# Performance work log

Hardware: AMD Instinct MI355X
Metric: run time of the kernel (lower is better)

The kernel has to match this reference:

```python
import jax, jax.numpy as jnp
import numpy as np

COMMITMENT_COST = 0.25
NUM_EMBEDDINGS = 8192
EMBEDDING_DIM = 64


def setup_inputs() -> dict:
    key = jax.random.key(0)
    k1, k2 = jax.random.split(key)
    z_e = jax.random.normal(k1, (32, 1024, EMBEDDING_DIM), dtype=jnp.float32)
    # nn.Embedding init: uniform(-1/num_embeddings, 1/num_embeddings)
    lim = 1.0 / NUM_EMBEDDINGS
    weight = jax.random.uniform(k2, (NUM_EMBEDDINGS, EMBEDDING_DIM), dtype=jnp.float32,
                                minval=-lim, maxval=lim)
    return {"z_e": z_e, "weight": weight}


def reference(z_e, weight):
    B = z_e.shape[0]
    D = weight.shape[1]
    z_flat = z_e.reshape(-1, D)  # [T, D], T = B*N
    # squared euclidean distances: ||z||^2 + ||e||^2 - 2 z e^T  -> [T, K]
    distances = (jnp.sum(z_flat ** 2, axis=1, keepdims=True)
                 + jnp.sum(weight ** 2, axis=1)
                 - 2.0 * jnp.matmul(z_flat, weight.T))
    encoding_indices = jnp.argmin(distances, axis=1)  # [T]
    # direct gather == one-hot @ weight (same math, no dense one-hot)
    z_q = weight[encoding_indices].reshape(z_e.shape)
    loss_1 = jnp.mean((jax.lax.stop_gradient(z_e) - z_q) ** 2)
    loss_2 = jnp.mean((z_e - jax.lax.stop_gradient(z_q)) ** 2)
    vq_loss = loss_1 + COMMITMENT_COST * loss_2
    # straight-through estimator
    z_q_st = z_e + jax.lax.stop_gradient(z_q - z_e)
    return (z_q_st, vq_loss)
```

## Files before the change

### kernel.cpp

```cpp
#include <hip/hip_runtime.h>

typedef float f32x16 __attribute__((ext_vector_type(16)));

#define NUM_EMB 8192
#define DIM 64
#define NTOK 32768
#define TOKS_PER_BLOCK 64
#define TOK_BLOCKS 512
#define ESPLIT 4
#define CHUNKS_PER_WAVE 16

#define B_SCALE (-8192.0f)
#define SCORE_BIAS 128.0f

#define WSB_OFF  0
#define WSA_OFF  (512 * 1024)
#define GKEY_OFF (WSA_OFF + 2 * 1024 * 1024)
#define CNT_OFF  (GKEY_OFF + 128 * 1024)
#define CNT2_OFF (CNT_OFF + 2048)
#define LOSSW_OFF (CNT2_OFF + 4)

__device__ __forceinline__ unsigned umin2(unsigned a, unsigned b) { return a < b ? a : b; }

__global__ __launch_bounds__(256) void vq_prep(const float* __restrict__ z_e,
                                               const float* __restrict__ weight,
                                               uint4* __restrict__ wsB,
                                               uint2* __restrict__ wsA,
                                               unsigned* __restrict__ gkeys,
                                               unsigned* __restrict__ cnt,
                                               unsigned* __restrict__ cnt2,
                                               float* __restrict__ lossw) {
  int m = blockIdx.x * 256 + threadIdx.x;
  if (m < TOK_BLOCKS)
    __hip_atomic_store(&cnt[m], 0u, __ATOMIC_RELAXED, __HIP_MEMORY_SCOPE_AGENT);
  if (m == TOK_BLOCKS) {
    __hip_atomic_store(cnt2, 0u, __ATOMIC_RELAXED, __HIP_MEMORY_SCOPE_AGENT);
    __hip_atomic_store(lossw, 0.0f, __ATOMIC_RELAXED, __HIP_MEMORY_SCOPE_AGENT);
  }
  if (m < NUM_EMB * 4) {
    __hip_atomic_store(&gkeys[m], 0xFFFFFFFFu, __ATOMIC_RELAXED, __HIP_MEMORY_SCOPE_AGENT);
    int lane = m & 63, h = (m >> 6) & 1, c = m >> 7;
    int n = c * 32 + (lane & 31);
    int kb = (lane >> 5) * 8;
    const float* p = weight + n * DIM;
    unsigned r[4];
#pragma unroll
    for (int q = 0; q < 2; ++q) {
      const float* pk = p + (2 * h + q) * 16 + kb;
      int lo = __builtin_amdgcn_cvt_pk_fp8_f32(B_SCALE * pk[0], B_SCALE * pk[1], 0, false);
      lo     = __builtin_amdgcn_cvt_pk_fp8_f32(B_SCALE * pk[2], B_SCALE * pk[3], lo, true);
      int hi = __builtin_amdgcn_cvt_pk_fp8_f32(B_SCALE * pk[4], B_SCALE * pk[5], 0, false);
      hi     = __builtin_amdgcn_cvt_pk_fp8_f32(B_SCALE * pk[6], B_SCALE * pk[7], hi, true);
      r[q * 2] = (unsigned)lo; r[q * 2 + 1] = (unsigned)hi;
    }
    wsB[m] = make_uint4(r[0], r[1], r[2], r[3]);
  } else {
    int s = m - NUM_EMB * 4;
    int lane = s & 63, f = (s >> 6) & 3, tr = (s >> 8) & 1, tile = s >> 9;
    int token = tile * 64 + tr * 32 + (lane & 31);
    const float* p = z_e + (size_t)token * DIM + f * 16 + (lane >> 5) * 8;
    int lo = __builtin_amdgcn_cvt_pk_fp8_f32(p[0], p[1], 0, false);
    lo     = __builtin_amdgcn_cvt_pk_fp8_f32(p[2], p[3], lo, true);
    int hi = __builtin_amdgcn_cvt_pk_fp8_f32(p[4], p[5], 0, false);
    hi     = __builtin_amdgcn_cvt_pk_fp8_f32(p[6], p[7], hi, true);
    wsA[s] = make_uint2((unsigned)lo, (unsigned)hi);
  }
}

__global__ __launch_bounds__(256, 4) void vq_main(const float* __restrict__ z_e,
                                                  const float* __restrict__ weight,
                                                  const uint2* __restrict__ wsA,
                                                  const uint4* __restrict__ wsB,
                                                  unsigned* __restrict__ gkeys,
                                                  unsigned* __restrict__ cnt,
                                                  unsigned* __restrict__ cnt2,
                                                  float* __restrict__ lossw,
                                                  float* __restrict__ out,
                                                  float* __restrict__ loss_out) {
  __shared__ unsigned lds_part[4][64];
  __shared__ unsigned lds_tok[64];
  __shared__ float wsum[4];
  __shared__ int winner;
  __shared__ int final_blk;

  const int tid  = threadIdx.x;
  const int lane = tid & 63;
  const int wave = tid >> 6;
  const int half = lane >> 5;
  const int ln31 = lane & 31;
  const int tblk = blockIdx.x & (TOK_BLOCKS - 1);
  const int eblk = blockIdx.x >> 9;
  const int tbase = tblk * TOKS_PER_BLOCK;

  long long afrag[2][4];
#pragma unroll
  for (int tr = 0; tr < 2; ++tr)
#pragma unroll
    for (int f = 0; f < 4; ++f) {
      uint2 u = wsA[(size_t)(((tblk * 2 + tr) * 4 + f) * 64 + lane)];
      __builtin_memcpy(&afrag[tr][f], &u, 8);
    }

  f32x16 bias;
#pragma unroll
  for (int i = 0; i < 16; ++i) bias[i] = SCORE_BIAS;

  unsigned run0[16], run1[16];
#pragma unroll
  for (int i = 0; i < 16; ++i) { run0[i] = 0xFFFFFFFFu; run1[i] = 0xFFFFFFFFu; }

  const int c0 = eblk * (CHUNKS_PER_WAVE * 4) + wave * CHUNKS_PER_WAVE;
  unsigned idx = (unsigned)(c0 * 32 + ln31);

  uint4 bA = wsB[(c0 * 2 + 0) * 64 + lane];
  uint4 bB = wsB[(c0 * 2 + 1) * 64 + lane];

  for (int c = 0; c < CHUNKS_PER_WAVE; ++c) {
    int cn = (c == CHUNKS_PER_WAVE - 1) ? c0 : (c0 + c + 1);
    uint4 nA = wsB[(cn * 2 + 0) * 64 + lane];
    uint4 nB = wsB[(cn * 2 + 1) * 64 + lane];

    long long b0, b1, b2, b3;
    __builtin_memcpy(&b0, &bA.x, 8);
    __builtin_memcpy(&b1, &bA.z, 8);
    __builtin_memcpy(&b2, &bB.x, 8);
    __builtin_memcpy(&b3, &bB.z, 8);

    f32x16 acc0 = __builtin_amdgcn_mfma_f32_32x32x16_fp8_fp8(afrag[0][0], b0, bias, 0, 0, 0);
    f32x16 acc1 = __builtin_amdgcn_mfma_f32_32x32x16_fp8_fp8(afrag[1][0], b0, bias, 0, 0, 0);
    acc0 = __builtin_amdgcn_mfma_f32_32x32x16_fp8_fp8(afrag[0][1], b1, acc0, 0, 0, 0);
    acc1 = __builtin_amdgcn_mfma_f32_32x32x16_fp8_fp8(afrag[1][1], b1, acc1, 0, 0, 0);
    acc0 = __builtin_amdgcn_mfma_f32_32x32x16_fp8_fp8(afrag[0][2], b2, acc0, 0, 0, 0);
    acc1 = __builtin_amdgcn_mfma_f32_32x32x16_fp8_fp8(afrag[1][2], b2, acc1, 0, 0, 0);
    acc0 = __builtin_amdgcn_mfma_f32_32x32x16_fp8_fp8(afrag[0][3], b3, acc0, 0, 0, 0);
    acc1 = __builtin_amdgcn_mfma_f32_32x32x16_fp8_fp8(afrag[1][3], b3, acc1, 0, 0, 0);

#pragma unroll
    for (int i = 0; i < 16; ++i) {
      run0[i] = umin2(run0[i], (__float_as_uint(acc0[i]) & 0xFFFFE000u) | idx);
      run1[i] = umin2(run1[i], (__float_as_uint(acc1[i]) & 0xFFFFE000u) | idx);
    }
    idx += 32;
    bA = nA; bB = nB;
  }

#pragma unroll
  for (int i = 0; i < 16; ++i) {
    unsigned v = run0[i];
    v = umin2(v, (unsigned)__builtin_amdgcn_ds_swizzle((int)v, 0x041F));
    v = umin2(v, (unsigned)__builtin_amdgcn_ds_swizzle((int)v, 0x081F));
    v = umin2(v, (unsigned)__builtin_amdgcn_ds_swizzle((int)v, 0x101F));
    v = umin2(v, (unsigned)__builtin_amdgcn_ds_swizzle((int)v, 0x201F));
    v = umin2(v, (unsigned)__builtin_amdgcn_ds_swizzle((int)v, 0x401F));
    run0[i] = v;
    unsigned w = run1[i];
    w = umin2(w, (unsigned)__builtin_amdgcn_ds_swizzle((int)w, 0x041F));
    w = umin2(w, (unsigned)__builtin_amdgcn_ds_swizzle((int)w, 0x081F));
    w = umin2(w, (unsigned)__builtin_amdgcn_ds_swizzle((int)w, 0x101F));
    w = umin2(w, (unsigned)__builtin_amdgcn_ds_swizzle((int)w, 0x201F));
    w = umin2(w, (unsigned)__builtin_amdgcn_ds_swizzle((int)w, 0x401F));
    run1[i] = w;
  }

  if (ln31 == 0) {
#pragma unroll
    for (int reg = 0; reg < 16; ++reg) {
      int rowl = (reg & 3) + 8 * (reg >> 2) + 4 * half;
      lds_part[wave][rowl]      = run0[reg];
      lds_part[wave][32 + rowl] = run1[reg];
    }
  }
  __syncthreads();

  if (tid < 64) {
    unsigned k = umin2(umin2(lds_part[0][tid], lds_part[1][tid]),
                       umin2(lds_part[2][tid], lds_part[3][tid]));
    atomicMin(&gkeys[tbase + tid], k);
  }
  __syncthreads();

  if (tid == 0) {
    unsigned prev = __hip_atomic_fetch_add(&cnt[tblk], 1u, __ATOMIC_RELAXED,
                                           __HIP_MEMORY_SCOPE_AGENT);
    winner = (prev == ESPLIT - 1);
  }
  __syncthreads();

  if (winner) {
    if (tid < 64)
      lds_tok[tid] = __hip_atomic_load(&gkeys[tbase + tid], __ATOMIC_RELAXED,
                                       __HIP_MEMORY_SCOPE_AGENT) & 0x1FFFu;
    __syncthreads();
    const float4* z4 = reinterpret_cast<const float4*>(z_e);
    const float4* w4 = reinterpret_cast<const float4*>(weight);
    float4* o4 = reinterpret_cast<float4*>(out);
    float lsum = 0.0f;
#pragma unroll
    for (int r = 0; r < 4; ++r) {
      int g = r * 256 + tid;
      int t = g >> 4, q = g & 15;
      float4 z = z4[(size_t)tbase * 16 + g];
      float4 w = w4[(size_t)lds_tok[t] * 16 + q];
      float4 o;
      o.x = z.x + (w.x - z.x); o.y = z.y + (w.y - z.y);
      o.z = z.z + (w.z - z.z); o.w = z.w + (w.w - z.w);
      o4[(size_t)tbase * 16 + g] = o;
      float dx = z.x - w.x, dy = z.y - w.y, dz = z.z - w.z, dw = z.w - w.w;
      lsum += dx * dx + dy * dy + dz * dz + dw * dw;
    }
#pragma unroll
    for (int s = 32; s >= 1; s >>= 1) lsum += __shfl_xor(lsum, s, 64);
    if (lane == 0) wsum[wave] = lsum;
    __syncthreads();
    if (tid == 0)
      atomicAdd(lossw, (wsum[0] + wsum[1] + wsum[2] + wsum[3]) * (1.25f / 2097152.0f));
    __syncthreads();
    if (tid == 0) {
      unsigned p2 = __hip_atomic_fetch_add(cnt2, 1u, __ATOMIC_RELAXED,
                                           __HIP_MEMORY_SCOPE_AGENT);
      final_blk = (p2 == TOK_BLOCKS - 1);
    }
    __syncthreads();
    if (final_blk && tid == 0)
      *loss_out = __hip_atomic_load(lossw, __ATOMIC_RELAXED, __HIP_MEMORY_SCOPE_AGENT);
  }
}

extern "C" void kernel_launch(void* const* d_in, const int* in_sizes, int n_in,
                              void* d_out, int out_size, void* d_ws, size_t ws_size,
                              hipStream_t stream) {
  const float* z_e    = (const float*)d_in[0];
  const float* weight = (const float*)d_in[1];
  float* out  = (float*)d_out;
  float* loss = out + (out_size - 1);
  char* ws = (char*)d_ws;
  uint4* wsB = (uint4*)(ws + WSB_OFF);
  uint2* wsA = (uint2*)(ws + WSA_OFF);
  unsigned* gkeys = (unsigned*)(ws + GKEY_OFF);
  unsigned* cnt   = (unsigned*)(ws + CNT_OFF);
  unsigned* cnt2  = (unsigned*)(ws + CNT2_OFF);
  float* lossw    = (float*)(ws + LOSSW_OFF);

  vq_prep<<<1152, 256, 0, stream>>>(z_e, weight, wsB, wsA, gkeys, cnt, cnt2, lossw);
  vq_main<<<TOK_BLOCKS * ESPLIT, 256, 0, stream>>>(z_e, weight, wsA, wsB, gkeys, cnt,
                                                   cnt2, lossw, out, loss);
}
```

Measured before the change: 107.6 us.

## Drop codebook split; each block scans full codebook for 32 tokens

```diff
diff --git a/kernel.cpp b/kernel.cpp
--- a/kernel.cpp
+++ b/kernel.cpp
@@ -5,111 +5,84 @@
 #define NUM_EMB 8192
 #define DIM 64
 #define NTOK 32768
-#define TOKS_PER_BLOCK 64
-#define TOK_BLOCKS 512
-#define ESPLIT 4
-#define CHUNKS_PER_WAVE 16
+#define TOKS_PER_BLOCK 32
+#define TOK_BLOCKS 1024
+#define CHUNKS_PER_WAVE 64
 
 #define B_SCALE (-8192.0f)
 #define SCORE_BIAS 128.0f
 
-#define WSB_OFF  0
-#define WSA_OFF  (512 * 1024)
-#define GKEY_OFF (WSA_OFF + 2 * 1024 * 1024)
-#define CNT_OFF  (GKEY_OFF + 128 * 1024)
-#define CNT2_OFF (CNT_OFF + 2048)
-#define LOSSW_OFF (CNT2_OFF + 4)
-
 __device__ __forceinline__ unsigned umin2(unsigned a, unsigned b) { return a < b ? a : b; }
 
-__global__ __launch_bounds__(256) void vq_prep(const float* __restrict__ z_e,
-                                               const float* __restrict__ weight,
+__global__ __launch_bounds__(256) void vq_prep(const float* __restrict__ weight,
                                                uint4* __restrict__ wsB,
-                                               uint2* __restrict__ wsA,
-                                               unsigned* __restrict__ gkeys,
-                                               unsigned* __restrict__ cnt,
-                                               unsigned* __restrict__ cnt2,
-                                               float* __restrict__ lossw) {
+                                               float* __restrict__ loss_out) {
   int m = blockIdx.x * 256 + threadIdx.x;
-  if (m < TOK_BLOCKS)
-    __hip_atomic_store(&cnt[m], 0u, __ATOMIC_RELAXED, __HIP_MEMORY_SCOPE_AGENT);
-  if (m == TOK_BLOCKS) {
-    __hip_atomic_store(cnt2, 0u, __ATOMIC_RELAXED, __HIP_MEMORY_SCOPE_AGENT);
-    __hip_atomic_store(lossw, 0.0f, __ATOMIC_RELAXED, __HIP_MEMORY_SCOPE_AGENT);
+  if (m == 0)
+    __hip_atomic_store(loss_out, 0.0f, __ATOMIC_RELAXED, __HIP_MEMORY_SCOPE_AGENT);
+  int lane = m & 63, h = (m >> 6) & 1, c = m >> 7;
+  int n = c * 32 + (lane & 31);
+  int kb = (lane >> 5) * 8;
+  const float* p = weight + n * DIM;
+  unsigned r[4];
+#pragma unroll
+  for (int q = 0; q < 2; ++q) {
+    const float* pk = p + (2 * h + q) * 16 + kb;
+    int lo = __builtin_amdgcn_cvt_pk_fp8_f32(B_SCALE * pk[0], B_SCALE * pk[1], 0, false);
+    lo     = __builtin_amdgcn_cvt_pk_fp8_f32(B_SCALE * pk[2], B_SCALE * pk[3], lo, true);
+    int hi = __builtin_amdgcn_cvt_pk_fp8_f32(B_SCALE * pk[4], B_SCALE * pk[5], 0, false);
+    hi     = __builtin_amdgcn_cvt_pk_fp8_f32(B_SCALE * pk[6], B_SCALE * pk[7], hi, true);
+    r[q * 2] = (unsigned)lo; r[q * 2 + 1] = (unsigned)hi;
   }
-  if (m < NUM_EMB * 4) {
-    __hip_atomic_store(&gkeys[m], 0xFFFFFFFFu, __ATOMIC_RELAXED, __HIP_MEMORY_SCOPE_AGENT);
-    int lane = m & 63, h = (m >> 6) & 1, c = m >> 7;
-    int n = c * 32 + (lane & 31);
-    int kb = (lane >> 5) * 8;
-    const float* p = weight + n * DIM;
-    unsigned r[4];
-#pragma unroll
-    for (int q = 0; q < 2; ++q) {
-      const float* pk = p + (2 * h + q) * 16 + kb;
-      int lo = __builtin_amdgcn_cvt_pk_fp8_f32(B_SCALE * pk[0], B_SCALE * pk[1], 0, false);
-      lo     = __builtin_amdgcn_cvt_pk_fp8_f32(B_SCALE * pk[2], B_SCALE * pk[3], lo, true);
-      int hi = __builtin_amdgcn_cvt_pk_fp8_f32(B_SCALE * pk[4], B_SCALE * pk[5], 0, false);
-      hi     = __builtin_amdgcn_cvt_pk_fp8_f32(B_SCALE * pk[6], B_SCALE * pk[7], hi, true);
-      r[q * 2] = (unsigned)lo; r[q * 2 + 1] = (unsigned)hi;
-    }
-    wsB[m] = make_uint4(r[0], r[1], r[2], r[3]);
-  } else {
-    int s = m - NUM_EMB * 4;
-    int lane = s & 63, f = (s >> 6) & 3, tr = (s >> 8) & 1, tile = s >> 9;
-    int token = tile * 64 + tr * 32 + (lane & 31);
-    const float* p = z_e + (size_t)token * DIM + f * 16 + (lane >> 5) * 8;
-    int lo = __builtin_amdgcn_cvt_pk_fp8_f32(p[0], p[1], 0, false);
-    lo     = __builtin_amdgcn_cvt_pk_fp8_f32(p[2], p[3], lo, true);
-    int hi = __builtin_amdgcn_cvt_pk_fp8_f32(p[4], p[5], 0, false);
-    hi     = __builtin_amdgcn_cvt_pk_fp8_f32(p[6], p[7], hi, true);
-    wsA[s] = make_uint2((unsigned)lo, (unsigned)hi);
-  }
+  wsB[m] = make_uint4(r[0], r[1], r[2], r[3]);
 }
 
 __global__ __launch_bounds__(256, 4) void vq_main(const float* __restrict__ z_e,
                                                   const float* __restrict__ weight,
-                                                  const uint2* __restrict__ wsA,
                                                   const uint4* __restrict__ wsB,
-                                                  unsigned* __restrict__ gkeys,
-                                                  unsigned* __restrict__ cnt,
-                                                  unsigned* __restrict__ cnt2,
-                                                  float* __restrict__ lossw,
                                                   float* __restrict__ out,
                                                   float* __restrict__ loss_out) {
-  __shared__ unsigned lds_part[4][64];
-  __shared__ unsigned lds_tok[64];
+  __shared__ unsigned char lds_a[TOKS_PER_BLOCK * 72];
+  __shared__ unsigned lds_part[4][TOKS_PER_BLOCK];
+  __shared__ unsigned lds_tok[TOKS_PER_BLOCK];
   __shared__ float wsum[4];
-  __shared__ int winner;
-  __shared__ int final_blk;
 
   const int tid  = threadIdx.x;
   const int lane = tid & 63;
   const int wave = tid >> 6;
   const int half = lane >> 5;
   const int ln31 = lane & 31;
-  const int tblk = blockIdx.x & (TOK_BLOCKS - 1);
-  const int eblk = blockIdx.x >> 9;
-  const int tbase = tblk * TOKS_PER_BLOCK;
+  const int tbase = blockIdx.x * TOKS_PER_BLOCK;
 
-  long long afrag[2][4];
+  {
+    int token = tid >> 3, g = tid & 7;
+    const float* p = z_e + (size_t)(tbase + token) * DIM + g * 8;
+    float4 x0 = *reinterpret_cast<const float4*>(p);
+    float4 x1 = *reinterpret_cast<const float4*>(p + 4);
+    int lo = __builtin_amdgcn_cvt_pk_fp8_f32(x0.x, x0.y, 0, false);
+    lo     = __builtin_amdgcn_cvt_pk_fp8_f32(x0.z, x0.w, lo, true);
+    int hi = __builtin_amdgcn_cvt_pk_fp8_f32(x1.x, x1.y, 0, false);
+    hi     = __builtin_amdgcn_cvt_pk_fp8_f32(x1.z, x1.w, hi, true);
+    *reinterpret_cast<uint2*>(&lds_a[token * 72 + g * 8]) = make_uint2((unsigned)lo, (unsigned)hi);
+  }
+  __syncthreads();
+
+  long long afrag[4];
 #pragma unroll
-  for (int tr = 0; tr < 2; ++tr)
-#pragma unroll
-    for (int f = 0; f < 4; ++f) {
-      uint2 u = wsA[(size_t)(((tblk * 2 + tr) * 4 + f) * 64 + lane)];
-      __builtin_memcpy(&afrag[tr][f], &u, 8);
-    }
+  for (int f = 0; f < 4; ++f) {
+    uint2 u = *reinterpret_cast<const uint2*>(&lds_a[ln31 * 72 + f * 16 + half * 8]);
+    __builtin_memcpy(&afrag[f], &u, 8);
+  }
 
   f32x16 bias;
 #pragma unroll
   for (int i = 0; i < 16; ++i) bias[i] = SCORE_BIAS;
 
-  unsigned run0[16], run1[16];
+  unsigned run[16];
 #pragma unroll
-  for (int i = 0; i < 16; ++i) { run0[i] = 0xFFFFFFFFu; run1[i] = 0xFFFFFFFFu; }
+  for (int i = 0; i < 16; ++i) run[i] = 0xFFFFFFFFu;
 
-  const int c0 = eblk * (CHUNKS_PER_WAVE * 4) + wave * CHUNKS_PER_WAVE;
+  const int c0 = wave * CHUNKS_PER_WAVE;
   unsigned idx = (unsigned)(c0 * 32 + ln31);
 
   uint4 bA = wsB[(c0 * 2 + 0) * 64 + lane];
@@ -126,104 +99,68 @@
     __builtin_memcpy(&b2, &bB.x, 8);
     __builtin_memcpy(&b3, &bB.z, 8);
 
-    f32x16 acc0 = __builtin_amdgcn_mfma_f32_32x32x16_fp8_fp8(afrag[0][0], b0, bias, 0, 0, 0);
-    f32x16 acc1 = __builtin_amdgcn_mfma_f32_32x32x16_fp8_fp8(afrag[1][0], b0, bias, 0, 0, 0);
-    acc0 = __builtin_amdgcn_mfma_f32_32x32x16_fp8_fp8(afrag[0][1], b1, acc0, 0, 0, 0);
-    acc1 = __builtin_amdgcn_mfma_f32_32x32x16_fp8_fp8(afrag[1][1], b1, acc1, 0, 0, 0);
-    acc0 = __builtin_amdgcn_mfma_f32_32x32x16_fp8_fp8(afrag[0][2], b2, acc0, 0, 0, 0);
-    acc1 = __builtin_amdgcn_mfma_f32_32x32x16_fp8_fp8(afrag[1][2], b2, acc1, 0, 0, 0);
-    acc0 = __builtin_amdgcn_mfma_f32_32x32x16_fp8_fp8(afrag[0][3], b3, acc0, 0, 0, 0);
-    acc1 = __builtin_amdgcn_mfma_f32_32x32x16_fp8_fp8(afrag[1][3], b3, acc1, 0, 0, 0);
+    f32x16 acc = __builtin_amdgcn_mfma_f32_32x32x16_fp8_fp8(afrag[0], b0, bias, 0, 0, 0);
+    acc = __builtin_amdgcn_mfma_f32_32x32x16_fp8_fp8(afrag[1], b1, acc, 0, 0, 0);
+    acc = __builtin_amdgcn_mfma_f32_32x32x16_fp8_fp8(afrag[2], b2, acc, 0, 0, 0);
+    acc = __builtin_amdgcn_mfma_f32_32x32x16_fp8_fp8(afrag[3], b3, acc, 0, 0, 0);
 
 #pragma unroll
-    for (int i = 0; i < 16; ++i) {
-      run0[i] = umin2(run0[i], (__float_as_uint(acc0[i]) & 0xFFFFE000u) | idx);
-      run1[i] = umin2(run1[i], (__float_as_uint(acc1[i]) & 0xFFFFE000u) | idx);
-    }
+    for (int i = 0; i < 16; ++i)
+      run[i] = umin2(run[i], (__float_as_uint(acc[i]) & 0xFFFFE000u) | idx);
     idx += 32;
     bA = nA; bB = nB;
   }
 
 #pragma unroll
   for (int i = 0; i < 16; ++i) {
-    unsigned v = run0[i];
+    unsigned v = run[i];
     v = umin2(v, (unsigned)__builtin_amdgcn_ds_swizzle((int)v, 0x041F));
     v = umin2(v, (unsigned)__builtin_amdgcn_ds_swizzle((int)v, 0x081F));
     v = umin2(v, (unsigned)__builtin_amdgcn_ds_swizzle((int)v, 0x101F));
     v = umin2(v, (unsigned)__builtin_amdgcn_ds_swizzle((int)v, 0x201F));
     v = umin2(v, (unsigned)__builtin_amdgcn_ds_swizzle((int)v, 0x401F));
-    run0[i] = v;
-    unsigned w = run1[i];
-    w = umin2(w, (unsigned)__builtin_amdgcn_ds_swizzle((int)w, 0x041F));
-    w = umin2(w, (unsigned)__builtin_amdgcn_ds_swizzle((int)w, 0x081F));
-    w = umin2(w, (unsigned)__builtin_amdgcn_ds_swizzle((int)w, 0x101F));
-    w = umin2(w, (unsigned)__builtin_amdgcn_ds_swizzle((int)w, 0x201F));
-    w = umin2(w, (unsigned)__builtin_amdgcn_ds_swizzle((int)w, 0x401F));
-    run1[i] = w;
+    run[i] = v;
   }
 
   if (ln31 == 0) {
 #pragma unroll
     for (int reg = 0; reg < 16; ++reg) {
-      int rowl = (reg & 3) + 8 * (reg >> 2) + 4 * half;
-      lds_part[wave][rowl]      = run0[reg];
-      lds_part[wave][32 + rowl] = run1[reg];
+      int row = (reg & 3) + 8 * (reg >> 2) + 4 * half;
+      lds_part[wave][row] = run[reg];
     }
   }
   __syncthreads();
 
-  if (tid < 64) {
+  if (tid < TOKS_PER_BLOCK) {
     unsigned k = umin2(umin2(lds_part[0][tid], lds_part[1][tid]),
                        umin2(lds_part[2][tid], lds_part[3][tid]));
-    atomicMin(&gkeys[tbase + tid], k);
+    lds_tok[tid] = k & 0x1FFFu;
   }
   __syncthreads();
 
-  if (tid == 0) {
-    unsigned prev = __hip_atomic_fetch_add(&cnt[tblk], 1u, __ATOMIC_RELAXED,
-                                           __HIP_MEMORY_SCOPE_AGENT);
-    winner = (prev == ESPLIT - 1);
+  const float4* z4 = reinterpret_cast<const float4*>(z_e);
+  const float4* w4 = reinterpret_cast<const float4*>(weight);
+  float4* o4 = reinterpret_cast<float4*>(out);
+  float lsum = 0.0f;
+#pragma unroll
+  for (int r = 0; r < 2; ++r) {
+    int g = r * 256 + tid;
+    int t = g >> 4, q = g & 15;
+    float4 z = z4[(size_t)tbase * 16 + g];
+    float4 w = w4[(size_t)lds_tok[t] * 16 + q];
+    float4 o;
+    o.x = z.x + (w.x - z.x); o.y = z.y + (w.y - z.y);
+    o.z = z.z + (w.z - z.z); o.w = z.w + (w.w - z.w);
+    o4[(size_t)tbase * 16 + g] = o;
+    float dx = z.x - w.x, dy = z.y - w.y, dz = z.z - w.z, dw = z.w - w.w;
+    lsum += dx * dx + dy * dy + dz * dz + dw * dw;
   }
+#pragma unroll
+  for (int s = 32; s >= 1; s >>= 1) lsum += __shfl_xor(lsum, s, 64);
+  if (lane == 0) wsum[wave] = lsum;
   __syncthreads();
-
-  if (winner) {
-    if (tid < 64)
-      lds_tok[tid] = __hip_atomic_load(&gkeys[tbase + tid], __ATOMIC_RELAXED,
-                                       __HIP_MEMORY_SCOPE_AGENT) & 0x1FFFu;
-    __syncthreads();
-    const float4* z4 = reinterpret_cast<const float4*>(z_e);
-    const float4* w4 = reinterpret_cast<const float4*>(weight);
-    float4* o4 = reinterpret_cast<float4*>(out);
-    float lsum = 0.0f;
-#pragma unroll
-    for (int r = 0; r < 4; ++r) {
-      int g = r * 256 + tid;
-      int t = g >> 4, q = g & 15;
-      float4 z = z4[(size_t)tbase * 16 + g];
-      float4 w = w4[(size_t)lds_tok[t] * 16 + q];
-      float4 o;
-      o.x = z.x + (w.x - z.x); o.y = z.y + (w.y - z.y);
-      o.z = z.z + (w.z - z.z); o.w = z.w + (w.w - z.w);
-      o4[(size_t)tbase * 16 + g] = o;
-      float dx = z.x - w.x, dy = z.y - w.y, dz = z.z - w.z, dw = z.w - w.w;
-      lsum += dx * dx + dy * dy + dz * dz + dw * dw;
-    }
-#pragma unroll
-    for (int s = 32; s >= 1; s >>= 1) lsum += __shfl_xor(lsum, s, 64);
-    if (lane == 0) wsum[wave] = lsum;
-    __syncthreads();
-    if (tid == 0)
-      atomicAdd(lossw, (wsum[0] + wsum[1] + wsum[2] + wsum[3]) * (1.25f / 2097152.0f));
-    __syncthreads();
-    if (tid == 0) {
-      unsigned p2 = __hip_atomic_fetch_add(cnt2, 1u, __ATOMIC_RELAXED,
-                                           __HIP_MEMORY_SCOPE_AGENT);
-      final_blk = (p2 == TOK_BLOCKS - 1);
-    }
-    __syncthreads();
-    if (final_blk && tid == 0)
-      *loss_out = __hip_atomic_load(lossw, __ATOMIC_RELAXED, __HIP_MEMORY_SCOPE_AGENT);
-  }
+  if (tid == 0)
+    atomicAdd(loss_out, (wsum[0] + wsum[1] + wsum[2] + wsum[3]) * (1.25f / 2097152.0f));
 }
 
 extern "C" void kernel_launch(void* const* d_in, const int* in_sizes, int n_in,
@@ -233,15 +170,8 @@
   const float* weight = (const float*)d_in[1];
   float* out  = (float*)d_out;
   float* loss = out + (out_size - 1);
-  char* ws = (char*)d_ws;
-  uint4* wsB = (uint4*)(ws + WSB_OFF);
-  uint2* wsA = (uint2*)(ws + WSA_OFF);
-  unsigned* gkeys = (unsigned*)(ws + GKEY_OFF);
-  unsigned* cnt   = (unsigned*)(ws + CNT_OFF);
-  unsigned* cnt2  = (unsigned*)(ws + CNT2_OFF);
-  float* lossw    = (float*)(ws + LOSSW_OFF);
+  uint4* wsB = (uint4*)d_ws;
 
-  vq_prep<<<1152, 256, 0, stream>>>(z_e, weight, wsB, wsA, gkeys, cnt, cnt2, lossw);
-  vq_main<<<TOK_BLOCKS * ESPLIT, 256, 0, stream>>>(z_e, weight, wsA, wsB, gkeys, cnt,
-                                                   cnt2, lossw, out, loss);
+  vq_prep<<<128, 256, 0, stream>>>(weight, wsB, loss);
+  vq_main<<<TOK_BLOCKS, 256, 0, stream>>>(z_e, weight, wsB, out, loss);
 }
```

Measured after the change: 103.9 us. 3.5% less time.
